# Performance work log

Measured on AMD Instinct MI355X. Metric: run time of the kernel, lower is better.

Reference implementation:

```python
import jax, jax.numpy as jnp
import numpy as np

N_NODES = 50000
N_EDGES = 2000000
H = 64            # hidden_channels
D_IN = 2 * H      # concat(src, dst)
NEG_SLOPE = 0.01  # torch F.leaky_relu default


def _mlp_params(key, scale=0.05):
    ks = jax.random.split(key, 8)
    dims = [(D_IN, H), (H, H), (H, H // 2), (H // 2, 1)]
    p = []
    for i, (din, dout) in enumerate(dims):
        p.append(jax.random.normal(ks[2 * i], (din, dout), jnp.float32) * scale)
        p.append(jax.random.normal(ks[2 * i + 1], (dout,), jnp.float32) * scale)
    return p


def setup_inputs() -> dict:
    key = jax.random.key(0)
    k1, k2, k3, ke, kw = jax.random.split(key, 5)
    x_src = jax.random.normal(k1, (N_NODES, H), jnp.float32)
    x_dst = jax.random.normal(k2, (N_NODES, H), jnp.float32)
    edge_label_index = jax.random.randint(k3, (2, N_EDGES), 0, N_NODES, jnp.int64)
    e = _mlp_params(ke)
    w = _mlp_params(kw)
    inp = {"x_src": x_src, "x_dst": x_dst, "edge_label_index": edge_label_index}
    for i in range(4):
        inp[f"ew{i+1}"] = e[2 * i]; inp[f"eb{i+1}"] = e[2 * i + 1]
        inp[f"ww{i+1}"] = w[2 * i]; inp[f"wb{i+1}"] = w[2 * i + 1]
    return inp


def _mlp(x, w1, b1, w2, b2, w3, b3, w4, b4):
    lrelu = lambda z: jax.nn.leaky_relu(z, NEG_SLOPE)
    x = lrelu(x @ w1 + b1)
    x = lrelu(x @ w2 + b2)
    x = lrelu(x @ w3 + b3)
    return x @ w4 + b4


def reference(x_src, x_dst, edge_label_index,
              ew1, eb1, ww1, wb1, ew2, eb2, ww2, wb2,
              ew3, eb3, ww3, wb3, ew4, eb4, ww4, wb4):
    # gather node features by edge endpoints, concat -> [E, 2H]
    combined = jnp.concatenate(
        [x_src[edge_label_index[0]], x_dst[edge_label_index[1]]], axis=-1)
    link_exists = _mlp(combined, ew1, eb1, ew2, eb2, ew3, eb3, ew4, eb4)
    link_weight = _mlp(combined, ww1, wb1, ww2, wb2, ww3, wb3, ww4, wb4)
    return link_exists, link_weight
```

## Files before the change

### kernel.cpp

```cpp
#include <hip/hip_runtime.h>


typedef _Float16 half8  __attribute__((ext_vector_type(8)));
typedef _Float16 half4v __attribute__((ext_vector_type(4)));
typedef _Float16 half2v __attribute__((ext_vector_type(2)));
typedef float    float4v __attribute__((ext_vector_type(4)));

#define MLP_W_BYTES 28672
#define MLP_R_BYTES 12288
#define W1F 0
#define W2F 16384
#define W3F 24576
#define LDS_TOTAL   16384
#define WS_REST_OFF 57344
#define WS_X16_OFF  81920

__device__ __forceinline__ float lrelu(float x) { return fmaxf(x, 0.01f * x); }

__device__ __forceinline__ int uperm(int k) {
    return 16 * (2 * ((k >> 2) & 1) + ((k >> 5) & 1)) + 4 * ((k >> 3) & 3) + (k & 3);
}

__global__ void prep_frags(const float* __restrict__ w1, const float* __restrict__ b1,
                           const float* __restrict__ w2, const float* __restrict__ b2,
                           const float* __restrict__ w3, const float* __restrict__ b3,
                           const float* __restrict__ w4,
                           unsigned char* __restrict__ dstL,
                           unsigned char* __restrict__ dstR)
{
    int idx = blockIdx.x * blockDim.x + threadIdx.x;
    if (idx < 8192) {
        int L = (idx >> 3) & 63, j = idx & 7, f = idx >> 9;
        int q = L >> 4, mm = L & 15, t = f >> 2, s = f & 3;
        int k = 32 * s + 8 * q + j;
        ((_Float16*)(dstL + W1F))[idx] = (_Float16)w1[k * 64 + 16 * t + mm];
        return;
    }
    idx -= 8192;
    if (idx < 4096) {
        int L = (idx >> 3) & 63, j = idx & 7, f = idx >> 9;
        int q = L >> 4, mm = L & 15, t = f >> 1, s = f & 1;
        int u = uperm(32 * s + 8 * q + j);
        ((_Float16*)(dstL + W2F))[idx] = (_Float16)w2[u * 64 + 16 * t + mm];
        return;
    }
    idx -= 4096;
    if (idx < 2048) {
        int L = (idx >> 3) & 63, j = idx & 7, f = idx >> 9;
        int q = L >> 4, mm = L & 15, t = f >> 1, s = f & 1;
        int u = uperm(32 * s + 8 * q + j);
        ((_Float16*)(dstL + W3F))[idx] = (_Float16)w3[u * 32 + 16 * t + mm];
        return;
    }
    idx -= 2048;
    if (idx < 512) {
        int L = idx >> 3, j = idx & 7;
        int q = L >> 4, t = j >> 2, r = j & 3;
        ((float*)(dstR + 0))[idx] = w4[16 * t + 4 * q + r];
        return;
    }
    idx -= 512;
    if (idx < 1024) {
        int t = idx >> 8, L = (idx >> 2) & 63, r = idx & 3, q = L >> 4;
        ((float*)(dstR + 2048))[idx] = b1[16 * t + 4 * q + r];
        return;
    }
    idx -= 1024;
    if (idx < 1024) {
        int t = idx >> 8, L = (idx >> 2) & 63, r = idx & 3, q = L >> 4;
        ((float*)(dstR + 6144))[idx] = b2[16 * t + 4 * q + r];
        return;
    }
    idx -= 1024;
    if (idx < 512) {
        int t = idx >> 8, L = (idx >> 2) & 63, r = idx & 3, q = L >> 4;
        ((float*)(dstR + 10240))[idx] = b3[16 * t + 4 * q + r];
        return;
    }
}

__global__ void prep_nodes(const float* __restrict__ xs, const float* __restrict__ xd,
                           _Float16* __restrict__ os, _Float16* __restrict__ od, int n4)
{
    int stride = gridDim.x * blockDim.x;
    for (int i = blockIdx.x * blockDim.x + threadIdx.x; i < n4; i += stride) {
        float4v a = ((const float4v*)xs)[i];
        float4v b = ((const float4v*)xd)[i];
        half4v ha, hb;
#pragma unroll
        for (int j = 0; j < 4; ++j) { ha[j] = (_Float16)a[j]; hb[j] = (_Float16)b[j]; }
        ((half4v*)os)[i] = ha;
        ((half4v*)od)[i] = hb;
    }
}

__device__ __forceinline__ half2v cvt_pk(float a, float b) {
    return __builtin_bit_cast(half2v, __builtin_amdgcn_cvt_pkrtz(a, b));
}

__device__ __forceinline__ half8 repack2(float4v lo, float4v hi) {
    half8 r;
#pragma unroll
    for (int j = 0; j < 2; ++j) {
        half2v a = cvt_pk(lo[2 * j], lo[2 * j + 1]);
        half2v sa = a * (_Float16)0.01f;
        half2v ma = __builtin_elementwise_max(a, sa);
        r[2 * j] = ma[0]; r[2 * j + 1] = ma[1];
        half2v b = cvt_pk(hi[2 * j], hi[2 * j + 1]);
        half2v sb = b * (_Float16)0.01f;
        half2v mb = __builtin_elementwise_max(b, sb);
        r[4 + 2 * j] = mb[0]; r[4 + 2 * j + 1] = mb[1];
    }
    return r;
}

__device__ __forceinline__ int2 load_eidx(const int* __restrict__ eidx,
                                          int nE, int tile, int n)
{
    int e = tile * 16 + n;
    int ec = e < nE ? e : nE - 1;
    return make_int2(eidx[ec], eidx[nE + ec]);
}

__device__ __forceinline__ void gather_tile(const _Float16* __restrict__ xs,
                                            const _Float16* __restrict__ xd,
                                            int2 sd, int q, int4* G)
{
    const char* rs = (const char*)(xs + (size_t)sd.x * 64);
    const char* rd = (const char*)(xd + (size_t)sd.y * 64);
    G[0] = *(const int4*)(rs + 16 * q);
    G[1] = *(const int4*)(rs + 64 + 16 * q);
    G[2] = *(const int4*)(rd + 16 * q);
    G[3] = *(const int4*)(rd + 64 + 16 * q);
}

__device__ __forceinline__ int4 warm_tile(const _Float16* __restrict__ xs,
                                          const _Float16* __restrict__ xd,
                                          int2 sd, int c)
{
    int idx = (c & 2) ? sd.y : sd.x;
    const char* base = (const char*)(((c & 2) ? xd : xs) + (size_t)idx * 64);
    return *(const int4*)(base + (c & 1) * 64);
}

__global__ __launch_bounds__(256, 2)
void edge_mlp_mfma(const unsigned char* __restrict__ ws,
                   const _Float16* __restrict__ xs, const _Float16* __restrict__ xd,
                   const int* __restrict__ eidx,
                   const float* __restrict__ eb4p, const float* __restrict__ wb4p,
                   float* __restrict__ out, int nE, int ntiles)
{
    __shared__ unsigned char lds[LDS_TOTAL];
    const int m = (blockIdx.x >> 3) & 1;
    const int bid = (blockIdx.x & 7) | ((blockIdx.x >> 4) << 3);
    const unsigned char* wbase = ws + m * MLP_W_BYTES;
    const unsigned char* rbase = ws + WS_REST_OFF + m * MLP_R_BYTES;
    {
        const uint4* s = (const uint4*)(wbase + W1F);
        uint4* d = (uint4*)lds;
        for (int i = threadIdx.x; i < LDS_TOTAL / 16; i += 256) d[i] = s[i];
    }

    const int lane = threadIdx.x & 63;
    const int q = lane >> 4, n = lane & 15;
    const int wid = (bid << 2) | (threadIdx.x >> 6);
    const int nwaves = gridDim.x << 1;
    const float b4s = m ? wb4p[0] : eb4p[0];
    float* __restrict__ outm = out + (m ? nE : 0);

    half8 w2f[8], w3f[4];
#pragma unroll
    for (int f = 0; f < 8; ++f)
        w2f[f] = *(const half8*)(wbase + W2F + (f * 64 + lane) * 16);
#pragma unroll
    for (int f = 0; f < 4; ++f)
        w3f[f] = *(const half8*)(wbase + W3F + (f * 64 + lane) * 16);
    float4v w40 = *(const float4v*)(rbase + 0 + lane * 32);
    float4v w41 = *(const float4v*)(rbase + 0 + lane * 32 + 16);
    float4v b1f[4], b2f[4], b3f[2];
#pragma unroll
    for (int t = 0; t < 4; ++t)
        b1f[t] = *(const float4v*)(rbase + 2048 + (t * 64 + lane) * 16);
#pragma unroll
    for (int t = 0; t < 4; ++t)
        b2f[t] = *(const float4v*)(rbase + 6144 + (t * 64 + lane) * 16);
#pragma unroll
    for (int t = 0; t < 2; ++t)
        b3f[t] = *(const float4v*)(rbase + 10240 + (t * 64 + lane) * 16);

    __syncthreads();

    int4 Gcur[4], Gnxt[4];
    int4 W0 = {0,0,0,0}, W1 = {0,0,0,0}, W2 = {0,0,0,0}, junk = {0,0,0,0};
    int2 I1 = {0,0}, I2 = {0,0}, I3 = {0,0};

    int tile = wid;
    if (tile < ntiles) {
        int t1 = tile + nwaves;     if (t1 >= ntiles) t1 = ntiles - 1;
        int t2 = tile + 2 * nwaves; if (t2 >= ntiles) t2 = ntiles - 1;
        int t3 = tile + 3 * nwaves; if (t3 >= ntiles) t3 = ntiles - 1;
        int2 I0 = load_eidx(eidx, nE, tile, n);
        I1 = load_eidx(eidx, nE, t1, n);
        I2 = load_eidx(eidx, nE, t2, n);
        I3 = load_eidx(eidx, nE, t3, n);
        W0 = warm_tile(xs, xd, I0, q);
        W1 = warm_tile(xs, xd, I1, q);
        W2 = warm_tile(xs, xd, I2, q);
        gather_tile(xs, xd, I0, q, Gcur);
    }

#pragma unroll 1
    for (; tile < ntiles; tile += nwaves) {
        half8 B1[4];
#pragma unroll
        for (int s = 0; s < 4; ++s) B1[s] = __builtin_bit_cast(half8, Gcur[s]);

        int tn = tile + nwaves;
        if (tn < ntiles)
            gather_tile(xs, xd, I1, q, Gnxt);

        junk.x ^= W0.x; junk.y ^= W0.y; junk.z ^= W0.z; junk.w ^= W0.w;
        W0 = W1; W1 = W2;
        W2 = warm_tile(xs, xd, I3, q);

        {
            int t4 = tile + 4 * nwaves; if (t4 >= ntiles) t4 = ntiles - 1;
            I1 = I2; I2 = I3;
            I3 = load_eidx(eidx, nE, t4, n);
        }

        float4v acc[4];
#pragma unroll
        for (int t = 0; t < 4; ++t) {
            acc[t] = b1f[t];
#pragma unroll
            for (int s = 0; s < 4; ++s) {
                half8 A = *(const half8*)(lds + W1F + ((t * 4 + s) * 64 + lane) * 16);
                acc[t] = __builtin_amdgcn_mfma_f32_16x16x32_f16(A, B1[s], acc[t], 0, 0, 0);
            }
        }

        half8 B2[2] = { repack2(acc[0], acc[2]), repack2(acc[1], acc[3]) };
        float4v acc2[4];
#pragma unroll
        for (int t = 0; t < 4; ++t) {
            acc2[t] = b2f[t];
#pragma unroll
            for (int s = 0; s < 2; ++s)
                acc2[t] = __builtin_amdgcn_mfma_f32_16x16x32_f16(w2f[t * 2 + s], B2[s], acc2[t], 0, 0, 0);
        }
        half8 B3[2] = { repack2(acc2[0], acc2[2]), repack2(acc2[1], acc2[3]) };
        float4v acc3[2];
#pragma unroll
        for (int t = 0; t < 2; ++t) {
            acc3[t] = b3f[t];
#pragma unroll
            for (int s = 0; s < 2; ++s)
                acc3[t] = __builtin_amdgcn_mfma_f32_16x16x32_f16(w3f[t * 2 + s], B3[s], acc3[t], 0, 0, 0);
        }
        float o = 0.f;
#pragma unroll
        for (int r = 0; r < 4; ++r) o = fmaf(lrelu(acc3[0][r]), w40[r], o);
#pragma unroll
        for (int r = 0; r < 4; ++r) o = fmaf(lrelu(acc3[1][r]), w41[r], o);
        o += __shfl_xor(o, 16, 64);
        o += __shfl_xor(o, 32, 64);

        int e = tile * 16 + n;
        if (q == 0 && e < nE)
            outm[e] = o + b4s;

#pragma unroll
        for (int s = 0; s < 4; ++s) Gcur[s] = Gnxt[s];
    }

    junk.x ^= W0.x ^ W1.x ^ W2.x;
    junk.y ^= W0.y ^ W1.y ^ W2.y;
    junk.z ^= W0.z ^ W1.z ^ W2.z;
    junk.w ^= W0.w ^ W1.w ^ W2.w;
    if (nE < 0 && (junk.x | junk.y | junk.z | junk.w) != 0)
        out[0] = -1.0f;
}

extern "C" void kernel_launch(void* const* d_in, const int* in_sizes, int n_in,
                              void* d_out, int out_size, void* d_ws, size_t ws_size,
                              hipStream_t stream)
{
    const float* x_src = (const float*)d_in[0];
    const float* x_dst = (const float*)d_in[1];
    const int*   eidx  = (const int*)d_in[2];
    const float* ew1 = (const float*)d_in[3];
    const float* eb1 = (const float*)d_in[4];
    const float* ww1 = (const float*)d_in[5];
    const float* wb1 = (const float*)d_in[6];
    const float* ew2 = (const float*)d_in[7];
    const float* eb2 = (const float*)d_in[8];
    const float* ww2 = (const float*)d_in[9];
    const float* wb2 = (const float*)d_in[10];
    const float* ww3 = (const float*)d_in[13];
    const float* ew3 = (const float*)d_in[11];
    const float* eb3 = (const float*)d_in[12];
    const float* wb3 = (const float*)d_in[14];
    const float* ew4 = (const float*)d_in[15];
    const float* eb4 = (const float*)d_in[16];
    const float* ww4 = (const float*)d_in[17];
    const float* wb4 = (const float*)d_in[18];
    float* out = (float*)d_out;

    const int nE = in_sizes[2] / 2;
    const int nNodeElems = in_sizes[0];
    unsigned char* ws = (unsigned char*)d_ws;
    _Float16* xs16 = (_Float16*)(ws + WS_X16_OFF);
    _Float16* xd16 = xs16 + nNodeElems;

    prep_frags<<<68, 256, 0, stream>>>(ew1, eb1, ew2, eb2, ew3, eb3, ew4,
                                       ws, ws + WS_REST_OFF);
    prep_frags<<<68, 256, 0, stream>>>(ww1, wb1, ww2, wb2, ww3, wb3, ww4,
                                       ws + MLP_W_BYTES, ws + WS_REST_OFF + MLP_R_BYTES);
    prep_nodes<<<1024, 256, 0, stream>>>(x_src, x_dst, xs16, xd16, nNodeElems / 4);

    const int ntiles = (nE + 15) / 16;
    edge_mlp_mfma<<<1024, 256, 0, stream>>>(ws, xs16, xd16, eidx, eb4, wb4,
                                            out, nE, ntiles);
}
```

Before: 295.1 us.

## Process two edge tiles per loop iteration with interleaved MFMA chains

The main loop now handles two 16-edge tiles (A and B) per iteration, interleaving their MFMA chains so the two independent dependency chains overlap and each LDS weight fragment load is shared by both tiles. The gather, warm-up and index prefetch pipeline is restructured to stay two tiles ahead. This aims to hide MFMA latency and halve per-tile LDS weight reads and loop overhead, at the cost of roughly doubled register pressure, which may lower occupancy. The clamp of prefetch tile indices to ntiles-1 is removed, so load_eidx must handle out-of-range tiles itself.

```diff
diff --git a/kernel.cpp b/kernel.cpp
--- a/kernel.cpp
+++ b/kernel.cpp
@@ -190,94 +190,116 @@
 
     __syncthreads();
 
-    int4 Gcur[4], Gnxt[4];
-    int4 W0 = {0,0,0,0}, W1 = {0,0,0,0}, W2 = {0,0,0,0}, junk = {0,0,0,0};
-    int2 I1 = {0,0}, I2 = {0,0}, I3 = {0,0};
+    int4 GcurA[4], GcurB[4], GnxtA[4], GnxtB[4];
+    int4 W0A = {0,0,0,0}, W0B = {0,0,0,0}, W1A = {0,0,0,0}, W1B = {0,0,0,0};
+    int4 junk = {0,0,0,0};
+    int2 I2 = {0,0}, I3 = {0,0}, I4 = {0,0}, I5 = {0,0};
 
     int tile = wid;
     if (tile < ntiles) {
-        int t1 = tile + nwaves;     if (t1 >= ntiles) t1 = ntiles - 1;
-        int t2 = tile + 2 * nwaves; if (t2 >= ntiles) t2 = ntiles - 1;
-        int t3 = tile + 3 * nwaves; if (t3 >= ntiles) t3 = ntiles - 1;
         int2 I0 = load_eidx(eidx, nE, tile, n);
-        I1 = load_eidx(eidx, nE, t1, n);
-        I2 = load_eidx(eidx, nE, t2, n);
-        I3 = load_eidx(eidx, nE, t3, n);
-        W0 = warm_tile(xs, xd, I0, q);
-        W1 = warm_tile(xs, xd, I1, q);
-        W2 = warm_tile(xs, xd, I2, q);
-        gather_tile(xs, xd, I0, q, Gcur);
+        int2 I1 = load_eidx(eidx, nE, tile + nwaves, n);
+        I2 = load_eidx(eidx, nE, tile + 2 * nwaves, n);
+        I3 = load_eidx(eidx, nE, tile + 3 * nwaves, n);
+        I4 = load_eidx(eidx, nE, tile + 4 * nwaves, n);
+        I5 = load_eidx(eidx, nE, tile + 5 * nwaves, n);
+        W0A = warm_tile(xs, xd, I0, q);
+        W0B = warm_tile(xs, xd, I1, q);
+        W1A = warm_tile(xs, xd, I2, q);
+        W1B = warm_tile(xs, xd, I3, q);
+        gather_tile(xs, xd, I0, q, GcurA);
+        gather_tile(xs, xd, I1, q, GcurB);
     }
 
 #pragma unroll 1
-    for (; tile < ntiles; tile += nwaves) {
-        half8 B1[4];
-#pragma unroll
-        for (int s = 0; s < 4; ++s) B1[s] = __builtin_bit_cast(half8, Gcur[s]);
-
-        int tn = tile + nwaves;
-        if (tn < ntiles)
-            gather_tile(xs, xd, I1, q, Gnxt);
-
-        junk.x ^= W0.x; junk.y ^= W0.y; junk.z ^= W0.z; junk.w ^= W0.w;
-        W0 = W1; W1 = W2;
-        W2 = warm_tile(xs, xd, I3, q);
-
-        {
-            int t4 = tile + 4 * nwaves; if (t4 >= ntiles) t4 = ntiles - 1;
-            I1 = I2; I2 = I3;
-            I3 = load_eidx(eidx, nE, t4, n);
-        }
-
-        float4v acc[4];
+    for (; tile < ntiles; tile += 2 * nwaves) {
+        half8 B1A[4], B1B[4];
+#pragma unroll
+        for (int s = 0; s < 4; ++s) {
+            B1A[s] = __builtin_bit_cast(half8, GcurA[s]);
+            B1B[s] = __builtin_bit_cast(half8, GcurB[s]);
+        }
+
+        gather_tile(xs, xd, I2, q, GnxtA);
+        gather_tile(xs, xd, I3, q, GnxtB);
+
+        junk.x ^= W0A.x ^ W0B.x; junk.y ^= W0A.y ^ W0B.y;
+        junk.z ^= W0A.z ^ W0B.z; junk.w ^= W0A.w ^ W0B.w;
+        W0A = W1A; W0B = W1B;
+        W1A = warm_tile(xs, xd, I4, q);
+        W1B = warm_tile(xs, xd, I5, q);
+
+        I2 = I4; I3 = I5;
+        I4 = load_eidx(eidx, nE, tile + 6 * nwaves, n);
+        I5 = load_eidx(eidx, nE, tile + 7 * nwaves, n);
+
+        float4v accA[4], accB[4];
 #pragma unroll
         for (int t = 0; t < 4; ++t) {
-            acc[t] = b1f[t];
+            accA[t] = b1f[t]; accB[t] = b1f[t];
 #pragma unroll
             for (int s = 0; s < 4; ++s) {
                 half8 A = *(const half8*)(lds + W1F + ((t * 4 + s) * 64 + lane) * 16);
-                acc[t] = __builtin_amdgcn_mfma_f32_16x16x32_f16(A, B1[s], acc[t], 0, 0, 0);
+                accA[t] = __builtin_amdgcn_mfma_f32_16x16x32_f16(A, B1A[s], accA[t], 0, 0, 0);
+                accB[t] = __builtin_amdgcn_mfma_f32_16x16x32_f16(A, B1B[s], accB[t], 0, 0, 0);
             }
         }
 
-        half8 B2[2] = { repack2(acc[0], acc[2]), repack2(acc[1], acc[3]) };
-        float4v acc2[4];
+        half8 B2A[2] = { repack2(accA[0], accA[2]), repack2(accA[1], accA[3]) };
+        half8 B2B[2] = { repack2(accB[0], accB[2]), repack2(accB[1], accB[3]) };
+        float4v acc2A[4], acc2B[4];
 #pragma unroll
         for (int t = 0; t < 4; ++t) {
-            acc2[t] = b2f[t];
-#pragma unroll
-            for (int s = 0; s < 2; ++s)
-                acc2[t] = __builtin_amdgcn_mfma_f32_16x16x32_f16(w2f[t * 2 + s], B2[s], acc2[t], 0, 0, 0);
-        }
-        half8 B3[2] = { repack2(acc2[0], acc2[2]), repack2(acc2[1], acc2[3]) };
-        float4v acc3[2];
+            acc2A[t] = b2f[t]; acc2B[t] = b2f[t];
+#pragma unroll
+            for (int s = 0; s < 2; ++s) {
+                acc2A[t] = __builtin_amdgcn_mfma_f32_16x16x32_f16(w2f[t * 2 + s], B2A[s], acc2A[t], 0, 0, 0);
+                acc2B[t] = __builtin_amdgcn_mfma_f32_16x16x32_f16(w2f[t * 2 + s], B2B[s], acc2B[t], 0, 0, 0);
+            }
+        }
+        half8 B3A[2] = { repack2(acc2A[0], acc2A[2]), repack2(acc2A[1], acc2A[3]) };
+        half8 B3B[2] = { repack2(acc2B[0], acc2B[2]), repack2(acc2B[1], acc2B[3]) };
+        float4v acc3A[2], acc3B[2];
 #pragma unroll
         for (int t = 0; t < 2; ++t) {
-            acc3[t] = b3f[t];
-#pragma unroll
-            for (int s = 0; s < 2; ++s)
-                acc3[t] = __builtin_amdgcn_mfma_f32_16x16x32_f16(w3f[t * 2 + s], B3[s], acc3[t], 0, 0, 0);
-        }
-        float o = 0.f;
-#pragma unroll
-        for (int r = 0; r < 4; ++r) o = fmaf(lrelu(acc3[0][r]), w40[r], o);
-#pragma unroll
-        for (int r = 0; r < 4; ++r) o = fmaf(lrelu(acc3[1][r]), w41[r], o);
-        o += __shfl_xor(o, 16, 64);
-        o += __shfl_xor(o, 32, 64);
-
-        int e = tile * 16 + n;
-        if (q == 0 && e < nE)
-            outm[e] = o + b4s;
-
-#pragma unroll
-        for (int s = 0; s < 4; ++s) Gcur[s] = Gnxt[s];
-    }
-
-    junk.x ^= W0.x ^ W1.x ^ W2.x;
-    junk.y ^= W0.y ^ W1.y ^ W2.y;
-    junk.z ^= W0.z ^ W1.z ^ W2.z;
-    junk.w ^= W0.w ^ W1.w ^ W2.w;
+            acc3A[t] = b3f[t]; acc3B[t] = b3f[t];
+#pragma unroll
+            for (int s = 0; s < 2; ++s) {
+                acc3A[t] = __builtin_amdgcn_mfma_f32_16x16x32_f16(w3f[t * 2 + s], B3A[s], acc3A[t], 0, 0, 0);
+                acc3B[t] = __builtin_amdgcn_mfma_f32_16x16x32_f16(w3f[t * 2 + s], B3B[s], acc3B[t], 0, 0, 0);
+            }
+        }
+        float oA = 0.f, oB = 0.f;
+#pragma unroll
+        for (int r = 0; r < 4; ++r) {
+            oA = fmaf(lrelu(acc3A[0][r]), w40[r], oA);
+            oB = fmaf(lrelu(acc3B[0][r]), w40[r], oB);
+        }
+#pragma unroll
+        for (int r = 0; r < 4; ++r) {
+            oA = fmaf(lrelu(acc3A[1][r]), w41[r], oA);
+            oB = fmaf(lrelu(acc3B[1][r]), w41[r], oB);
+        }
+        oA += __shfl_xor(oA, 16, 64);
+        oA += __shfl_xor(oA, 32, 64);
+        oB += __shfl_xor(oB, 16, 64);
+        oB += __shfl_xor(oB, 32, 64);
+
+        if (q == 0) {
+            int eA = tile * 16 + n;
+            int eB = (tile + nwaves) * 16 + n;
+            if (eA < nE) outm[eA] = oA + b4s;
+            if (eB < nE) outm[eB] = oB + b4s;
+        }
+
+#pragma unroll
+        for (int s = 0; s < 4; ++s) { GcurA[s] = GnxtA[s]; GcurB[s] = GnxtB[s]; }
+    }
+
+    junk.x ^= W0A.x ^ W0B.x ^ W1A.x ^ W1B.x;
+    junk.y ^= W0A.y ^ W0B.y ^ W1A.y ^ W1B.y;
+    junk.z ^= W0A.z ^ W0B.z ^ W1A.z ^ W1B.z;
+    junk.w ^= W0A.w ^ W0B.w ^ W1A.w ^ W1B.w;
     if (nE < 0 && (junk.x | junk.y | junk.z | junk.w) != 0)
         out[0] = -1.0f;
 }
@@ -297,9 +319,9 @@
     const float* eb2 = (const float*)d_in[8];
     const float* ww2 = (const float*)d_in[9];
     const float* wb2 = (const float*)d_in[10];
-    const float* ww3 = (const float*)d_in[13];
     const float* ew3 = (const float*)d_in[11];
     const float* eb3 = (const float*)d_in[12];
+    const float* ww3 = (const float*)d_in[13];
     const float* wb3 = (const float*)d_in[14];
     const float* ew4 = (const float*)d_in[15];
     const float* eb4 = (const float*)d_in[16];
```

Result: slower. 362.2 us (+22.7%).
